# Performance work log

Hardware: AMD Instinct MI355X
Metric: run time of the kernel (lower is better)

## Reference

```python
import jax, jax.numpy as jnp
import numpy as np

B, T, D, H, MLP, WIN = 4, 2048, 768, 12, 3072, 256
HD = D // H


def setup_inputs() -> dict:
    key = jax.random.key(0)
    ks = jax.random.split(key, 9)
    s = 0.02
    return {
        "x": jax.random.normal(ks[0], (B, T, D), jnp.float32),
        "in_proj_w": jax.random.normal(ks[1], (3 * D, D), jnp.float32) * s,
        "in_proj_b": jax.random.normal(ks[2], (3 * D,), jnp.float32) * s,
        "out_w": jax.random.normal(ks[3], (D, D), jnp.float32) * s,
        "out_b": jax.random.normal(ks[4], (D,), jnp.float32) * s,
        "w1": jax.random.normal(ks[5], (MLP, D), jnp.float32) * s,
        "b1": jax.random.normal(ks[6], (MLP,), jnp.float32) * s,
        "w2": jax.random.normal(ks[7], (D, MLP), jnp.float32) * s,
        "b2": jax.random.normal(ks[8], (D,), jnp.float32) * s,
        "ln1_g": jnp.ones((D,), jnp.float32),
        "ln1_b": jnp.zeros((D,), jnp.float32),
        "ln2_g": jnp.ones((D,), jnp.float32),
        "ln2_b": jnp.zeros((D,), jnp.float32),
        "window_size": WIN,
    }


def _layernorm(v, g, b, eps=1e-5):
    m = v.mean(-1, keepdims=True)
    var = ((v - m) ** 2).mean(-1, keepdims=True)
    return (v - m) / jnp.sqrt(var + eps) * g + b


def reference(x, in_proj_w, in_proj_b, out_w, out_b, w1, b1, w2, b2,
              ln1_g, ln1_b, ln2_g, ln2_b, window_size):
    Bx, Tx, Dx = x.shape
    # --- local (banded) multi-head self-attention on norm1(x) ---
    xn = _layernorm(x, ln1_g, ln1_b)
    qkv = xn @ in_proj_w.T + in_proj_b            # [B,T,3D]
    q, k, v = jnp.split(qkv, 3, axis=-1)
    to_heads = lambda t: t.reshape(Bx, Tx, H, HD).transpose(0, 2, 1, 3)  # [B,H,T,hd]
    q, k, v = to_heads(q), to_heads(k), to_heads(v)
    scale = jnp.asarray(1.0 / np.sqrt(HD), x.dtype)
    scores = jnp.einsum('bhqd,bhkd->bhqk', q, k) * scale  # [B,H,T,T]
    idx = jnp.arange(Tx)
    banned = jnp.abs(idx[:, None] - idx[None, :]) > window_size  # True = masked
    scores = jnp.where(banned, -jnp.inf, scores)
    attn = jax.nn.softmax(scores, axis=-1)
    o = jnp.einsum('bhqk,bhkd->bhqd', attn, v)
    o = o.transpose(0, 2, 1, 3).reshape(Bx, Tx, Dx)
    o = o @ out_w.T + out_b
    x = x + o
    # --- MLP block on norm2(x) ---
    xn = _layernorm(x, ln2_g, ln2_b)
    h = jax.nn.gelu(xn @ w1.T + b1, approximate=False)
    x = x + (h @ w2.T + b2)
    return x
```

## Files before the change

### kernel.cpp

```cpp
#include <hip/hip_runtime.h>
#include <hip/hip_bf16.h>

typedef __bf16 bf16;
typedef __bf16 v8bf __attribute__((ext_vector_type(8)));
typedef __bf16 v4bf __attribute__((ext_vector_type(4)));
typedef float  v4f  __attribute__((ext_vector_type(4)));

#define DEVI __device__ __forceinline__

constexpr int Bc   = 4;
constexpr int Tc   = 2048;
constexpr int Dc   = 768;
constexpr int Hc   = 12;
constexpr int HDc  = 64;
constexpr int MLPc = 3072;
constexpr int QKVc = 2304;
constexpr int BTc  = Bc * Tc;

DEVI float b2f(bf16 x) { return (float)x; }
DEVI bf16  f2b(float x) { return (bf16)x; }

#define GLDS(gp, lp) __builtin_amdgcn_global_load_lds( \
    (const __attribute__((address_space(1))) void*)(gp), \
    (__attribute__((address_space(3))) void*)(lp), 16, 0, 0)

__global__ __launch_bounds__(256) void cvt2_kernel(
    const float* __restrict__ s0, bf16* __restrict__ d0, int n0,
    const float* __restrict__ s1, bf16* __restrict__ d1)
{
    int i = blockIdx.x * 256 + threadIdx.x;
    const float* s; bf16* d; int j;
    if (i < n0) { s = s0; d = d0; j = i; }
    else        { s = s1; d = d1; j = i - n0; }
    float4 v = ((const float4*)s)[j];
    v4bf o = { f2b(v.x), f2b(v.y), f2b(v.z), f2b(v.w) };
    ((v4bf*)d)[j] = o;
}

__global__ __launch_bounds__(256) void ln_kernel(
    const float* __restrict__ x, const float* __restrict__ g,
    const float* __restrict__ bt, bf16* __restrict__ out)
{
    const int row = blockIdx.x;
    const int t = threadIdx.x;
    const float* xr = x + (size_t)row * Dc;
    float v[3];
    v[0] = xr[t];
    v[1] = xr[t + 256];
    v[2] = xr[t + 512];
    float s = v[0] + v[1] + v[2];
    float s2 = v[0]*v[0] + v[1]*v[1] + v[2]*v[2];
    #pragma unroll
    for (int off = 32; off > 0; off >>= 1) {
        s  += __shfl_down(s, off);
        s2 += __shfl_down(s2, off);
    }
    __shared__ float red[8];
    const int wave = t >> 6, lane = t & 63;
    if (lane == 0) { red[wave] = s; red[4 + wave] = s2; }
    __syncthreads();
    s  = red[0] + red[1] + red[2] + red[3];
    s2 = red[4] + red[5] + red[6] + red[7];
    const float mean = s * (1.0f / Dc);
    const float var  = s2 * (1.0f / Dc) - mean * mean;
    const float rstd = rsqrtf(var + 1e-5f);
    bf16* orow = out + (size_t)row * Dc;
    #pragma unroll
    for (int i = 0; i < 3; i++) {
        int c = t + i * 256;
        orow[c] = f2b((v[i] - mean) * rstd * g[c] + bt[c]);
    }
}

enum { EPI_QKV = 0, EPI_GELU_BF16 = 1, EPI_RESID_F32 = 2, EPI_ACC_F32 = 3 };

template <int EPI, int TN, int BK>
__global__ __launch_bounds__(256) void gemm_bt(
    const bf16* __restrict__ A, const bf16* __restrict__ Bw,
    const float* __restrict__ bias,
    bf16* __restrict__ Cb, float* __restrict__ Cf,
    const float* __restrict__ resf,
    int M, int N, int K, int lda, int ldb)
{
    constexpr int MI = (TN == 128) ? 4 : 2;
    constexpr int CH = BK / 8;
    __shared__ __align__(16) bf16 sA[128 * BK];
    __shared__ __align__(16) bf16 sB[TN * BK];
    const int t = threadIdx.x, wave = t >> 6, lane = t & 63;
    const int moff = (TN == 128) ? (wave & 1) * 64 : wave * 32;
    const int noff = (TN == 128) ? (wave >> 1) * 64 : 0;
    const int nx = gridDim.x, ny = gridDim.y;
    const int bid = blockIdx.y * nx + blockIdx.x;
    const int xcd = bid & 7, kk = bid >> 3;
    const int m0 = (xcd * (ny >> 3) + kk / nx) * 128;
    const int n0 = (kk % nx) * TN;
    const bf16* Ag = A + (size_t)m0 * lda;
    const bf16* Bg = Bw + (size_t)n0 * ldb;

    v4f acc[MI][4];
    #pragma unroll
    for (int i = 0; i < MI; i++)
        #pragma unroll
        for (int j = 0; j < 4; j++) acc[i][j] = (v4f)(0.0f);

    for (int k0 = 0; k0 < K; k0 += BK) {
        #pragma unroll
        for (int i = 0; i < (128 * CH) / 256; i++) {
            int c = i * 256 + t;
            int r = c / CH, l0 = c % CH;
            int j = ((l0 & 7) ^ (r & 7)) | (l0 & ~7);
            GLDS(Ag + (size_t)r * lda + k0 + j * 8,
                 &sA[(i * 256 + wave * 64) * 8]);
        }
        #pragma unroll
        for (int i = 0; i < (TN * CH) / 256; i++) {
            int c = i * 256 + t;
            int r = c / CH, l0 = c % CH;
            int j = ((l0 & 7) ^ (r & 7)) | (l0 & ~7);
            GLDS(Bg + (size_t)r * ldb + k0 + j * 8,
                 &sB[(i * 256 + wave * 64) * 8]);
        }
        __syncthreads();
        #pragma unroll
        for (int ks = 0; ks < BK / 32; ks++) {
            const int rq = lane >> 4, rl = lane & 15;
            const int q = ks * 4 + rq;
            v8bf a[MI], b[4];
            #pragma unroll
            for (int mi = 0; mi < MI; mi++) {
                const int row = moff + mi * 16 + rl;
                const int l = ((q & 7) ^ (row & 7)) | (q & ~7);
                a[mi] = *(const v8bf*)&sA[row * BK + l * 8];
            }
            #pragma unroll
            for (int ni = 0; ni < 4; ni++) {
                const int row = noff + ni * 16 + rl;
                const int l = ((q & 7) ^ (row & 7)) | (q & ~7);
                b[ni] = *(const v8bf*)&sB[row * BK + l * 8];
            }
            #pragma unroll
            for (int mi = 0; mi < MI; mi++)
                #pragma unroll
                for (int ni = 0; ni < 4; ni++)
                    acc[mi][ni] = __builtin_amdgcn_mfma_f32_16x16x32_bf16(
                        a[mi], b[ni], acc[mi][ni], 0, 0, 0);
        }
        __syncthreads();
    }

    const int rq = lane >> 4, cn = lane & 15;
    #pragma unroll
    for (int mi = 0; mi < MI; mi++)
        #pragma unroll
        for (int ni = 0; ni < 4; ni++) {
            const int col = n0 + noff + ni * 16 + cn;
            const float bv = bias ? bias[col] : 0.0f;
            if constexpr (EPI == EPI_QKV) {
                const int row0 = m0 + moff + mi * 16 + rq * 4;
                if (n0 < 2 * Dc) {
                    bf16* dst = Cb + (col < Dc ? 0 : (size_t)BTc * Dc);
                    const int cadj = col < Dc ? col : col - Dc;
                    const float qs = (col < Dc) ? 0.18033688011112042f : 1.0f;
                    #pragma unroll
                    for (int r = 0; r < 4; r++)
                        dst[(size_t)(row0 + r) * Dc + cadj] = f2b((acc[mi][ni][r] + bv) * qs);
                } else {
                    const int vcol = col - 2 * Dc;
                    const int hh = vcol >> 6, hd = vcol & 63;
                    const int bb = row0 >> 11, t0 = row0 & 2047;
                    v4bf pk;
                    #pragma unroll
                    for (int r = 0; r < 4; r++) pk[r] = f2b(acc[mi][ni][r] + bv);
                    *(v4bf*)(Cb + 2 * (size_t)BTc * Dc +
                             (((size_t)bb * Hc + hh) * HDc + hd) * Tc + t0) = pk;
                }
            } else {
                #pragma unroll
                for (int r = 0; r < 4; r++) {
                    const int row = m0 + moff + mi * 16 + rq * 4 + r;
                    const size_t idx = (size_t)row * N + col;
                    float vv = acc[mi][ni][r] + bv;
                    if constexpr (EPI == EPI_GELU_BF16) {
                        Cb[idx] = f2b(0.5f * vv * (1.0f + erff(vv * 0.70710678118f)));
                    } else if constexpr (EPI == EPI_RESID_F32) {
                        Cf[idx] = vv + resf[idx];
                    } else {
                        Cf[idx] = vv + Cf[idx];
                    }
                }
            }
        }
}

__global__ __launch_bounds__(256, 3) void attn_kernel(
    const bf16* __restrict__ Qb, const bf16* __restrict__ Kb,
    const bf16* __restrict__ Vt, bf16* __restrict__ o,
    const int* __restrict__ winp)
{
    const int bh = blockIdx.x, qt = blockIdx.y;
    const int b = bh / Hc, h = bh % Hc;
    const int q0 = qt * 128;
    const int win = *winp;
    const int t = threadIdx.x, wave = t >> 6, lane = t & 63;
    const int rq = lane >> 4, cn = lane & 15;
    const int qw0 = q0 + wave * 32;

    __shared__ __align__(16) bf16 sK[64 * 64];
    __shared__ __align__(16) bf16 sV[64 * 64];
    __shared__ __align__(16) bf16 sP[4][32 * 64];
    bf16* const sPw = &sP[wave][0];
    const int swz = (cn & 7) << 1;

    const bf16* qp  = Qb + ((size_t)b * Tc) * Dc + h * HDc;
    const bf16* kp  = Kb + ((size_t)b * Tc) * Dc + h * HDc;
    const bf16* vtp = Vt + (size_t)bh * HDc * Tc;

    v8bf qf[2][2];
    #pragma unroll
    for (int ks = 0; ks < 2; ks++)
        #pragma unroll
        for (int mi = 0; mi < 2; mi++)
            qf[ks][mi] = *(const v8bf*)(qp + (size_t)(qw0 + mi * 16 + cn) * Dc
                                        + ks * 32 + rq * 8);

    v4f acc_o[2][4];
    #pragma unroll
    for (int mi = 0; mi < 2; mi++)
        #pragma unroll
        for (int nh = 0; nh < 4; nh++) acc_o[mi][nh] = (v4f)(0.0f);
    float l_part[2] = {0.0f, 0.0f};

    const int wlo = max(0, qw0 - win), whi = min(Tc - 1, qw0 + 31 + win);
    const int klo = max(0, q0 - win) & ~63;
    const int khi = min(Tc - 1, q0 + 127 + win);

    for (int kb0 = klo; kb0 <= khi; kb0 += 64) {
        #pragma unroll
        for (int i = 0; i < 2; i++) {
            int c = i * 256 + t;
            int r = c >> 3, j = (c & 7) ^ (r & 7);
            GLDS(kp + (size_t)(kb0 + r) * Dc + j * 8,
                 &sK[(i * 256 + wave * 64) * 8]);
            GLDS(vtp + (size_t)r * Tc + kb0 + j * 8,
                 &sV[(i * 256 + wave * 64) * 8]);
        }
        __syncthreads();

        if (kb0 + 63 >= wlo && kb0 <= whi) {
            v4f sf[4][2];
            #pragma unroll
            for (int kb = 0; kb < 4; kb++)
                #pragma unroll
                for (int mi = 0; mi < 2; mi++) sf[kb][mi] = (v4f)(0.0f);
            #pragma unroll
            for (int ks = 0; ks < 2; ks++) {
                v8bf kf[4];
                #pragma unroll
                for (int kb = 0; kb < 4; kb++) {
                    const int row = kb * 16 + cn;
                    kf[kb] = *(const v8bf*)&sK[row * 64
                                              + ((ks * 4 + rq) ^ (row & 7)) * 8];
                }
                #pragma unroll
                for (int kb = 0; kb < 4; kb++)
                    #pragma unroll
                    for (int mi = 0; mi < 2; mi++)
                        sf[kb][mi] = __builtin_amdgcn_mfma_f32_16x16x32_bf16(
                            kf[kb], qf[ks][mi], sf[kb][mi], 0, 0, 0);
            }

            const bool need_mask = (kb0 + 63 - qw0 > win) || (qw0 + 31 - kb0 > win);
            #pragma unroll
            for (int kb = 0; kb < 4; kb++)
                #pragma unroll
                for (int mi = 0; mi < 2; mi++) {
                    v4bf pk;
                    #pragma unroll
                    for (int r = 0; r < 4; r++) {
                        float tt = sf[kb][mi][r];
                        if (need_mask) {
                            int ki = kb0 + kb * 16 + rq * 4 + r;
                            int qi = qw0 + mi * 16 + cn;
                            int dd = qi - ki; dd = dd < 0 ? -dd : dd;
                            tt = (dd > win) ? -INFINITY : tt;
                        }
                        float p = exp2f(fminf(tt, 30.0f));
                        l_part[mi] += p;
                        pk[r] = f2b(p);
                    }
                    *(v4bf*)&sPw[(mi * 16 + cn) * 64
                                 + (((kb * 4 + rq) ^ swz) << 2)] = pk;
                }

            #pragma unroll
            for (int ks = 0; ks < 2; ks++) {
                v8bf pa[2], vf[4];
                #pragma unroll
                for (int mi = 0; mi < 2; mi++)
                    pa[mi] = *(const v8bf*)&sPw[(mi * 16 + cn) * 64
                                                + (((ks * 8 + rq * 2) ^ swz) << 2)];
                #pragma unroll
                for (int nh = 0; nh < 4; nh++) {
                    const int row = nh * 16 + cn;
                    vf[nh] = *(const v8bf*)&sV[row * 64
                                               + ((ks * 4 + rq) ^ (row & 7)) * 8];
                }
                #pragma unroll
                for (int mi = 0; mi < 2; mi++)
                    #pragma unroll
                    for (int nh = 0; nh < 4; nh++)
                        acc_o[mi][nh] = __builtin_amdgcn_mfma_f32_16x16x32_bf16(
                            pa[mi], vf[nh], acc_o[mi][nh], 0, 0, 0);
            }
        }
        __syncthreads();
    }

    #pragma unroll
    for (int mi = 0; mi < 2; mi++) {
        l_part[mi] += __shfl_xor(l_part[mi], 16);
        l_part[mi] += __shfl_xor(l_part[mi], 32);
    }

    bf16* ob = o + ((size_t)b * Tc + qw0) * Dc + h * HDc;
    #pragma unroll
    for (int mi = 0; mi < 2; mi++)
        #pragma unroll
        for (int r = 0; r < 4; r++) {
            const float lv = __shfl(l_part[mi], rq * 4 + r);
            const float invl = 1.0f / lv;
            #pragma unroll
            for (int nh = 0; nh < 4; nh++)
                ob[(size_t)(mi * 16 + rq * 4 + r) * Dc + nh * 16 + cn] =
                    f2b(acc_o[mi][nh][r] * invl);
        }
}

extern "C" void kernel_launch(void* const* d_in, const int* in_sizes, int n_in,
                              void* d_out, int out_size, void* d_ws, size_t ws_size,
                              hipStream_t stream)
{
    const float* x     = (const float*)d_in[0];
    const float* inw   = (const float*)d_in[1];
    const float* inb   = (const float*)d_in[2];
    const float* outw  = (const float*)d_in[3];
    const float* outb  = (const float*)d_in[4];
    const float* w1    = (const float*)d_in[5];
    const float* b1    = (const float*)d_in[6];
    const float* w2    = (const float*)d_in[7];
    const float* b2    = (const float*)d_in[8];
    const float* ln1g  = (const float*)d_in[9];
    const float* ln1b  = (const float*)d_in[10];
    const float* ln2g  = (const float*)d_in[11];
    const float* ln2b  = (const float*)d_in[12];
    const int*   winp  = (const int*)d_in[13];
    float* out = (float*)d_out;

    char* ws = (char*)d_ws;
    constexpr size_t A_OFF   = 0;
    constexpr size_t QKV_OFF = (size_t)BTc * Dc * 2;
    constexpr size_t WA_OFF  = QKV_OFF + 3 * (size_t)BTc * Dc * 2;
    constexpr size_t WS_NEED = WA_OFF + (size_t)(QKVc + Dc) * Dc * 2;
    if (ws_size < WS_NEED) return;

    bf16*  xn     = (bf16*)(ws + A_OFF);
    bf16*  qkvb   = (bf16*)(ws + QKV_OFF);
    bf16*  Qb     = qkvb;
    bf16*  Kb     = qkvb + (size_t)BTc * Dc;
    bf16*  Vt     = qkvb + 2 * (size_t)BTc * Dc;
    bf16*  hbuf   = (bf16*)(ws + QKV_OFF);
    bf16*  wmlp   = (bf16*)(ws + QKV_OFF + (size_t)BTc * (2 * Dc) * 2);
    bf16*  w1_b   = wmlp;
    bf16*  w2_b   = wmlp + (size_t)MLPc * Dc;
    bf16*  wqkv_b = (bf16*)(ws + WA_OFF);
    bf16*  wout_b = wqkv_b + (size_t)QKVc * Dc;

    constexpr int MHALF = BTc / 2;
    constexpr int NQKV4 = QKVc * Dc / 4, NOUT4 = Dc * Dc / 4;
    constexpr int NW14  = MLPc * Dc / 4, NW24  = Dc * MLPc / 4;

    cvt2_kernel<<<(NQKV4 + NOUT4) / 256, 256, 0, stream>>>(
        inw, wqkv_b, NQKV4, outw, wout_b);

    ln_kernel<<<BTc, 256, 0, stream>>>(x, ln1g, ln1b, xn);
    gemm_bt<EPI_QKV, 128, 64><<<dim3(QKVc / 128, BTc / 128), 256, 0, stream>>>(
        xn, wqkv_b, inb, qkvb, nullptr, nullptr, BTc, QKVc, Dc, Dc, Dc);
    attn_kernel<<<dim3(Bc * Hc, Tc / 128), 256, 0, stream>>>(Qb, Kb, Vt, xn, winp);
    cvt2_kernel<<<(NW14 + NW24) / 256, 256, 0, stream>>>(
        w1, w1_b, NW14, w2, w2_b);
    gemm_bt<EPI_RESID_F32, 64, 128><<<dim3(Dc / 64, BTc / 128), 256, 0, stream>>>(
        xn, wout_b, outb, nullptr, out, x, BTc, Dc, Dc, Dc, Dc);
    ln_kernel<<<BTc, 256, 0, stream>>>(out, ln2g, ln2b, xn);

    for (int r = 0; r < 2; r++) {
        const bf16* xnr = xn + (size_t)r * MHALF * Dc;
        float*      outr = out + (size_t)r * MHALF * Dc;
        gemm_bt<EPI_GELU_BF16, 128, 64><<<dim3(MLPc / 128, MHALF / 128), 256, 0, stream>>>(
            xnr, w1_b, b1, hbuf, nullptr, nullptr, MHALF, MLPc, Dc, Dc, Dc);
        gemm_bt<EPI_ACC_F32, 64, 128><<<dim3(Dc / 64, MHALF / 128), 256, 0, stream>>>(
            hbuf, w2_b, b2, nullptr, outr, nullptr, MHALF, Dc, MLPc, MLPc, MLPc);
    }
}
```

Baseline: 381.7 us.

## Double-buffer LDS tiles in GEMM and attention kernels with async prefetch

Adds two-stage LDS buffers to the GEMM and attention kernels, issuing the next tile's global-to-LDS loads before computing on the current tile and waiting with explicit vmcnt counts plus raw barriers. The goal is to hide global memory latency behind MFMA work. It also changes the block-to-tile mapping so consecutive blocks on an XCD walk M first, and reduces BK to 64 for the narrow GEMMs so the doubled LDS footprint still fits. Doubling LDS use may lower occupancy, and the hand-written vmcnt counts must match the actual number of issued loads.

```diff
diff --git a/kernel.cpp b/kernel.cpp
--- a/kernel.cpp
+++ b/kernel.cpp
@@ -84,43 +84,60 @@
 {
     constexpr int MI = (TN == 128) ? 4 : 2;
     constexpr int CH = BK / 8;
-    __shared__ __align__(16) bf16 sA[128 * BK];
-    __shared__ __align__(16) bf16 sB[TN * BK];
+    constexpr int AI = (128 * CH) / 256;
+    constexpr int BI = (TN * CH) / 256;
+    constexpr int NST = AI + BI;
+    __shared__ __align__(16) bf16 sA[2][128 * BK];
+    __shared__ __align__(16) bf16 sB[2][TN * BK];
     const int t = threadIdx.x, wave = t >> 6, lane = t & 63;
     const int moff = (TN == 128) ? (wave & 1) * 64 : wave * 32;
     const int noff = (TN == 128) ? (wave >> 1) * 64 : 0;
     const int nx = gridDim.x, ny = gridDim.y;
+    const int nym = ny >> 3;
     const int bid = blockIdx.y * nx + blockIdx.x;
     const int xcd = bid & 7, kk = bid >> 3;
-    const int m0 = (xcd * (ny >> 3) + kk / nx) * 128;
-    const int n0 = (kk % nx) * TN;
+    const int m0 = (xcd * nym + kk % nym) * 128;
+    const int n0 = (kk / nym) * TN;
     const bf16* Ag = A + (size_t)m0 * lda;
     const bf16* Bg = Bw + (size_t)n0 * ldb;
 
-    v4f acc[MI][4];
-    #pragma unroll
-    for (int i = 0; i < MI; i++)
-        #pragma unroll
-        for (int j = 0; j < 4; j++) acc[i][j] = (v4f)(0.0f);
-
-    for (int k0 = 0; k0 < K; k0 += BK) {
-        #pragma unroll
-        for (int i = 0; i < (128 * CH) / 256; i++) {
+    auto stage = [&](int pb, int k0) {
+        #pragma unroll
+        for (int i = 0; i < AI; i++) {
             int c = i * 256 + t;
             int r = c / CH, l0 = c % CH;
             int j = ((l0 & 7) ^ (r & 7)) | (l0 & ~7);
             GLDS(Ag + (size_t)r * lda + k0 + j * 8,
-                 &sA[(i * 256 + wave * 64) * 8]);
-        }
-        #pragma unroll
-        for (int i = 0; i < (TN * CH) / 256; i++) {
+                 &sA[pb][(i * 256 + wave * 64) * 8]);
+        }
+        #pragma unroll
+        for (int i = 0; i < BI; i++) {
             int c = i * 256 + t;
             int r = c / CH, l0 = c % CH;
             int j = ((l0 & 7) ^ (r & 7)) | (l0 & ~7);
             GLDS(Bg + (size_t)r * ldb + k0 + j * 8,
-                 &sB[(i * 256 + wave * 64) * 8]);
-        }
-        __syncthreads();
+                 &sB[pb][(i * 256 + wave * 64) * 8]);
+        }
+    };
+
+    v4f acc[MI][4];
+    #pragma unroll
+    for (int i = 0; i < MI; i++)
+        #pragma unroll
+        for (int j = 0; j < 4; j++) acc[i][j] = (v4f)(0.0f);
+
+    int cur = 0;
+    stage(0, 0);
+    for (int k0 = 0; k0 < K; k0 += BK) {
+        if (k0 + BK < K) {
+            stage(cur ^ 1, k0 + BK);
+            asm volatile("s_waitcnt vmcnt(%0)" :: "n"(NST) : "memory");
+        } else {
+            asm volatile("s_waitcnt vmcnt(0)" ::: "memory");
+        }
+        __builtin_amdgcn_s_barrier();
+        const bf16* cA = sA[cur];
+        const bf16* cB = sB[cur];
         #pragma unroll
         for (int ks = 0; ks < BK / 32; ks++) {
             const int rq = lane >> 4, rl = lane & 15;
@@ -130,13 +147,13 @@
             for (int mi = 0; mi < MI; mi++) {
                 const int row = moff + mi * 16 + rl;
                 const int l = ((q & 7) ^ (row & 7)) | (q & ~7);
-                a[mi] = *(const v8bf*)&sA[row * BK + l * 8];
+                a[mi] = *(const v8bf*)&cA[row * BK + l * 8];
             }
             #pragma unroll
             for (int ni = 0; ni < 4; ni++) {
                 const int row = noff + ni * 16 + rl;
                 const int l = ((q & 7) ^ (row & 7)) | (q & ~7);
-                b[ni] = *(const v8bf*)&sB[row * BK + l * 8];
+                b[ni] = *(const v8bf*)&cB[row * BK + l * 8];
             }
             #pragma unroll
             for (int mi = 0; mi < MI; mi++)
@@ -145,7 +162,8 @@
                     acc[mi][ni] = __builtin_amdgcn_mfma_f32_16x16x32_bf16(
                         a[mi], b[ni], acc[mi][ni], 0, 0, 0);
         }
-        __syncthreads();
+        __builtin_amdgcn_s_barrier();
+        cur ^= 1;
     }
 
     const int rq = lane >> 4, cn = lane & 15;
@@ -205,8 +223,8 @@
     const int rq = lane >> 4, cn = lane & 15;
     const int qw0 = q0 + wave * 32;
 
-    __shared__ __align__(16) bf16 sK[64 * 64];
-    __shared__ __align__(16) bf16 sV[64 * 64];
+    __shared__ __align__(16) bf16 sK[2][64 * 64];
+    __shared__ __align__(16) bf16 sV[2][64 * 64];
     __shared__ __align__(16) bf16 sP[4][32 * 64];
     bf16* const sPw = &sP[wave][0];
     const int swz = (cn & 7) << 1;
@@ -215,6 +233,18 @@
     const bf16* kp  = Kb + ((size_t)b * Tc) * Dc + h * HDc;
     const bf16* vtp = Vt + (size_t)bh * HDc * Tc;
 
+    auto stage_kv = [&](int pb, int kb) {
+        #pragma unroll
+        for (int i = 0; i < 2; i++) {
+            int c = i * 256 + t;
+            int r = c >> 3, j = (c & 7) ^ (r & 7);
+            GLDS(kp + (size_t)(kb + r) * Dc + j * 8,
+                 &sK[pb][(i * 256 + wave * 64) * 8]);
+            GLDS(vtp + (size_t)r * Tc + kb + j * 8,
+                 &sV[pb][(i * 256 + wave * 64) * 8]);
+        }
+    };
+
     v8bf qf[2][2];
     #pragma unroll
     for (int ks = 0; ks < 2; ks++)
@@ -234,19 +264,20 @@
     const int klo = max(0, q0 - win) & ~63;
     const int khi = min(Tc - 1, q0 + 127 + win);
 
+    int cur = 0;
+    stage_kv(0, klo);
     for (int kb0 = klo; kb0 <= khi; kb0 += 64) {
-        #pragma unroll
-        for (int i = 0; i < 2; i++) {
-            int c = i * 256 + t;
-            int r = c >> 3, j = (c & 7) ^ (r & 7);
-            GLDS(kp + (size_t)(kb0 + r) * Dc + j * 8,
-                 &sK[(i * 256 + wave * 64) * 8]);
-            GLDS(vtp + (size_t)r * Tc + kb0 + j * 8,
-                 &sV[(i * 256 + wave * 64) * 8]);
-        }
-        __syncthreads();
+        if (kb0 + 64 <= khi) {
+            stage_kv(cur ^ 1, kb0 + 64);
+            asm volatile("s_waitcnt vmcnt(4)" ::: "memory");
+        } else {
+            asm volatile("s_waitcnt vmcnt(0)" ::: "memory");
+        }
+        __builtin_amdgcn_s_barrier();
 
         if (kb0 + 63 >= wlo && kb0 <= whi) {
+            const bf16* cK = sK[cur];
+            const bf16* cV = sV[cur];
             v4f sf[4][2];
             #pragma unroll
             for (int kb = 0; kb < 4; kb++)
@@ -258,7 +289,7 @@
                 #pragma unroll
                 for (int kb = 0; kb < 4; kb++) {
                     const int row = kb * 16 + cn;
-                    kf[kb] = *(const v8bf*)&sK[row * 64
+                    kf[kb] = *(const v8bf*)&cK[row * 64
                                               + ((ks * 4 + rq) ^ (row & 7)) * 8];
                 }
                 #pragma unroll
@@ -302,7 +333,7 @@
                 #pragma unroll
                 for (int nh = 0; nh < 4; nh++) {
                     const int row = nh * 16 + cn;
-                    vf[nh] = *(const v8bf*)&sV[row * 64
+                    vf[nh] = *(const v8bf*)&cV[row * 64
                                                + ((ks * 4 + rq) ^ (row & 7)) * 8];
                 }
                 #pragma unroll
@@ -313,7 +344,8 @@
                             pa[mi], vf[nh], acc_o[mi][nh], 0, 0, 0);
             }
         }
-        __syncthreads();
+        __builtin_amdgcn_s_barrier();
+        cur ^= 1;
     }
 
     #pragma unroll
@@ -388,7 +420,7 @@
     attn_kernel<<<dim3(Bc * Hc, Tc / 128), 256, 0, stream>>>(Qb, Kb, Vt, xn, winp);
     cvt2_kernel<<<(NW14 + NW24) / 256, 256, 0, stream>>>(
         w1, w1_b, NW14, w2, w2_b);
-    gemm_bt<EPI_RESID_F32, 64, 128><<<dim3(Dc / 64, BTc / 128), 256, 0, stream>>>(
+    gemm_bt<EPI_RESID_F32, 64, 64><<<dim3(Dc / 64, BTc / 128), 256, 0, stream>>>(
         xn, wout_b, outb, nullptr, out, x, BTc, Dc, Dc, Dc, Dc);
     ln_kernel<<<BTc, 256, 0, stream>>>(out, ln2g, ln2b, xn);
 
@@ -397,7 +429,7 @@
         float*      outr = out + (size_t)r * MHALF * Dc;
         gemm_bt<EPI_GELU_BF16, 128, 64><<<dim3(MLPc / 128, MHALF / 128), 256, 0, stream>>>(
             xnr, w1_b, b1, hbuf, nullptr, nullptr, MHALF, MLPc, Dc, Dc, Dc);
-        gemm_bt<EPI_ACC_F32, 64, 128><<<dim3(Dc / 64, MHALF / 128), 256, 0, stream>>>(
+        gemm_bt<EPI_ACC_F32, 64, 64><<<dim3(Dc / 64, MHALF / 128), 256, 0, stream>>>(
             hbuf, w2_b, b2, nullptr, outr, nullptr, MHALF, Dc, MLPc, MLPc, MLPc);
     }
 }
```

Result: slower. 420.9 us (+10.3%).
